# Performance work log

Measured on AMD Instinct MI355X. Metric: run time of the kernel, lower is better.

The kernel has to match this reference:

```python
import jax, jax.numpy as jnp
import numpy as np

EMBED = 256; HEADS = 8; LEVELS = 4; POINTS = 4; HEAD_DIM = EMBED // HEADS
B = 2; Q = 20000; HP = 128; WP = 128
EPS = 1e-5


def setup_inputs() -> dict:
    key = jax.random.key(0)
    ks = jax.random.split(key, 12)
    s = 1.0 / np.sqrt(EMBED)
    return {
        "query": jax.random.normal(ks[0], (Q, EMBED), jnp.float32),
        "query_spatial_positions": jax.random.uniform(ks[1], (Q, 2), jnp.float32),
        "query_batch_offsets": jnp.array([0, Q // 2, Q], dtype=jnp.int32),
        "stacked_feature_maps": jax.random.normal(ks[2], (B, HP, WP, LEVELS, EMBED), jnp.float32),
        "level_spatial_shapes": jnp.array([[128, 128], [64, 64], [32, 32], [16, 16]], dtype=jnp.int32),
        "norm_gamma": jnp.ones((EMBED,), jnp.float32),
        "norm_beta": jnp.zeros((EMBED,), jnp.float32),
        "W_q": jax.random.normal(ks[3], (EMBED, EMBED), jnp.float32) * s,
        "W_off": jax.random.normal(ks[4], (EMBED, HEADS * LEVELS * POINTS * 2), jnp.float32) * s * 0.1,
        "b_off": jax.random.normal(ks[5], (HEADS * LEVELS * POINTS * 2,), jnp.float32) * 0.5,
        "W_attn": jax.random.normal(ks[6], (EMBED, HEADS * LEVELS * POINTS), jnp.float32) * s,
        "b_attn": jnp.zeros((HEADS * LEVELS * POINTS,), jnp.float32),
        "W_val": jax.random.normal(ks[7], (EMBED, EMBED), jnp.float32) * s,
        "b_val": jnp.zeros((EMBED,), jnp.float32),
        "W_out": jax.random.normal(ks[8], (EMBED, EMBED), jnp.float32) * s,
    }


def _layernorm(x, g, b):
    mu = x.mean(-1, keepdims=True)
    xc = x - mu
    v = (xc * xc).mean(-1, keepdims=True)
    return xc * jax.lax.rsqrt(v + EPS) * g + b


def reference(query, query_spatial_positions, query_batch_offsets, stacked_feature_maps,
              level_spatial_shapes, norm_gamma, norm_beta, W_q, W_off, b_off,
              W_attn, b_attn, W_val, b_val, W_out):
    residual = query
    x = _layernorm(query, norm_gamma, norm_beta)
    x = x @ W_q  # q_in_proj (no bias)

    off = (x @ W_off + b_off).reshape(Q, HEADS, LEVELS, POINTS, 2)
    attn = jax.nn.softmax((x @ W_attn + b_attn).reshape(Q, HEADS, LEVELS * POINTS), axis=-1)
    attn = attn.reshape(Q, HEADS, LEVELS, POINTS)

    # value projection over all levels, split into heads: [B,HP,WP,L,H,HD]
    value = (stacked_feature_maps @ W_val + b_val).reshape(B, HP, WP, LEVELS, HEADS, HEAD_DIM)

    shp = level_spatial_shapes.astype(jnp.float32)  # [L,2] (h,w)
    # normalized ref point + offset scaled by level size -> pixel coords (align_corners=False)
    loc = query_spatial_positions[:, None, None, None, :] + off / shp[None, None, :, None, :]
    pix = loc * shp[None, None, :, None, :] - 0.5  # [Q,H,L,P,2]
    py, px = pix[..., 0], pix[..., 1]
    y0 = jnp.floor(py); x0 = jnp.floor(px)
    wy = py - y0; wx = px - x0
    y0i = y0.astype(jnp.int32); x0i = x0.astype(jnp.int32)

    Hl = level_spatial_shapes[:, 0][None, None, :, None]
    Wl = level_spatial_shapes[:, 1][None, None, :, None]
    b_idx = (jnp.searchsorted(query_batch_offsets, jnp.arange(Q, dtype=jnp.int32), side='right') - 1)[:, None, None, None]
    l_idx = jnp.arange(LEVELS)[None, None, :, None]
    h_idx = jnp.arange(HEADS)[None, :, None, None]

    def gather(yi, xi, w):
        m = (yi >= 0) & (yi < Hl) & (xi >= 0) & (xi < Wl)  # zero-pad outside level extent
        yc = jnp.clip(yi, 0, HP - 1)
        xc = jnp.clip(xi, 0, WP - 1)
        v = value[b_idx, yc, xc, l_idx, h_idx]  # [Q,H,L,P,HD]
        return v * (w * m)[..., None]

    samp = (gather(y0i, x0i, (1 - wy) * (1 - wx))
            + gather(y0i, x0i + 1, (1 - wy) * wx)
            + gather(y0i + 1, x0i, wy * (1 - wx))
            + gather(y0i + 1, x0i + 1, wy * wx))

    out = (attn[..., None] * samp).sum(axis=(2, 3)).reshape(Q, EMBED)
    return out @ W_out + residual
```

## Files before the change

kernel.cpp:

```cpp
#include <hip/hip_runtime.h>
#include <hip/hip_bf16.h>
#include <stdint.h>

#define EMBED 256
#define HEADS 8
#define LEVELS 4
#define POINTS 4
#define HEAD_DIM 32
#define HPAD 128
#define WPAD 128
#define LN_EPS 1e-5f

typedef unsigned short u16;
typedef __attribute__((ext_vector_type(8))) short bf16x8v;
typedef __attribute__((ext_vector_type(4))) float f32x4;

static __device__ __forceinline__ float bu2f(u16 u) {
  return __uint_as_float(((unsigned)u) << 16);
}
static __device__ __forceinline__ u16 f2bu(float f) {
  unsigned x = __float_as_uint(f);
  return (u16)((x + 0x7fffu + ((x >> 16) & 1u)) >> 16);
}
static __device__ __forceinline__ float loadf(const void* p, size_t i, int isbf) {
  return isbf ? bu2f(((const u16*)p)[i]) : ((const float*)p)[i];
}
static __device__ __forceinline__ int imin(int a, int b) { return a < b ? a : b; }

static __device__ __forceinline__ void cp16(const u16* g, u16* l) {
  __builtin_amdgcn_global_load_lds((const __attribute__((address_space(1))) unsigned*)g,
                                   (__attribute__((address_space(3))) unsigned*)l, 16, 0, 0);
}

__global__ __launch_bounds__(256) void detect_kernel(const unsigned* __restrict__ q,
                                                     int* __restrict__ flag) {
  int t = threadIdx.x;
  __shared__ int s[256];
  unsigned u = q[t * 13 + 1];
  unsigned e = (u >> 7) & 0xFF;
  s[t] = (e >= 116 && e <= 130) ? 1 : 0;
  __syncthreads();
  for (int st = 128; st > 0; st >>= 1) { if (t < st) s[t] += s[t + st]; __syncthreads(); }
  if (t == 0) *flag = (s[0] > 200) ? 1 : 0;
}

__global__ __launch_bounds__(384) void boa_kernel(const void* __restrict__ b_off,
                                                  const void* __restrict__ b_attn,
                                                  float* __restrict__ boa,
                                                  const int* __restrict__ dflag) {
  int fl = *dflag;
  int t = threadIdx.x;
  boa[t] = (t < 256) ? loadf(b_off, t, fl) : loadf(b_attn, t - 256, fl);
}

__global__ __launch_bounds__(1024) void wcomb_kernel(const void* __restrict__ Wq,
                                                     const void* __restrict__ Woff,
                                                     const void* __restrict__ Wattn,
                                                     u16* __restrict__ Wt,
                                                     const int* __restrict__ dflag) {
  int fl = *dflag;
  int n0 = blockIdx.x * 32, k0 = blockIdx.y * 32;
  int tx = threadIdx.x & 31;
  int ty = threadIdx.x >> 5;
  __shared__ float Aq[32][33];
  __shared__ float Bo[32][33];
  float acc = 0.f;
  for (int j0 = 0; j0 < 256; j0 += 32) {
    Aq[ty][tx] = loadf(Wq, (size_t)(k0 + ty) * 256 + j0 + tx, fl);
    int n = n0 + tx;
    Bo[ty][tx] = (n < 256) ? loadf(Woff,  (size_t)(j0 + ty) * 256 + n,        fl)
                           : loadf(Wattn, (size_t)(j0 + ty) * 128 + (n - 256), fl);
    __syncthreads();
#pragma unroll
    for (int j = 0; j < 32; j++) acc += Aq[ty][j] * Bo[j][tx];
    __syncthreads();
  }
  Wt[(size_t)(n0 + tx) * 256 + k0 + ty] = f2bu(acc);
}

__global__ __launch_bounds__(256) void wtrans_kernel(const void* __restrict__ W,
                                                     u16* __restrict__ Wt,
                                                     int K, int N,
                                                     const int* __restrict__ dflag) {
  int fl = *dflag;
  __shared__ float tile[32][33];
  int tx = threadIdx.x & 31, ty = threadIdx.x >> 5;
  int k0 = blockIdx.x * 32, n0 = blockIdx.y * 32;
#pragma unroll
  for (int j = 0; j < 4; j++) {
    int r = ty + j * 8;
    tile[r][tx] = loadf(W, (size_t)(k0 + r) * N + n0 + tx, fl);
  }
  __syncthreads();
#pragma unroll
  for (int j = 0; j < 4; j++) {
    int n = ty + j * 8;
    Wt[(size_t)(n0 + n) * K + k0 + tx] = f2bu(tile[tx][n]);
  }
}

__global__ __launch_bounds__(256) void ln_kernel(const void* __restrict__ q,
                                                 const void* __restrict__ g,
                                                 const void* __restrict__ be,
                                                 u16* __restrict__ out, int Qn,
                                                 const int* __restrict__ dflag) {
  int fl = *dflag;
  int row = blockIdx.x * 4 + (threadIdx.x >> 6);
  int lane = threadIdx.x & 63;
  if (row >= Qn) return;
  float v0, v1, v2, v3;
  if (fl) {
    uint2 u = *(const uint2*)((const u16*)q + (size_t)row * 256 + lane * 4);
    v0 = bu2f((u16)(u.x & 0xffff)); v1 = bu2f((u16)(u.x >> 16));
    v2 = bu2f((u16)(u.y & 0xffff)); v3 = bu2f((u16)(u.y >> 16));
  } else {
    float4 f = *(const float4*)((const float*)q + (size_t)row * 256 + lane * 4);
    v0 = f.x; v1 = f.y; v2 = f.z; v3 = f.w;
  }
  float s = v0 + v1 + v2 + v3;
#pragma unroll
  for (int m = 1; m < 64; m <<= 1) s += __shfl_xor(s, m, 64);
  float mu = s * (1.f / 256.f);
  float c0 = v0 - mu, c1 = v1 - mu, c2 = v2 - mu, c3 = v3 - mu;
  float s2 = c0 * c0 + c1 * c1 + c2 * c2 + c3 * c3;
#pragma unroll
  for (int m = 1; m < 64; m <<= 1) s2 += __shfl_xor(s2, m, 64);
  float r = rsqrtf(s2 * (1.f / 256.f) + LN_EPS);
  float o0 = c0 * r * loadf(g, lane * 4 + 0, fl) + loadf(be, lane * 4 + 0, fl);
  float o1 = c1 * r * loadf(g, lane * 4 + 1, fl) + loadf(be, lane * 4 + 1, fl);
  float o2 = c2 * r * loadf(g, lane * 4 + 2, fl) + loadf(be, lane * 4 + 2, fl);
  float o3 = c3 * r * loadf(g, lane * 4 + 3, fl) + loadf(be, lane * 4 + 3, fl);
  uint2 w;
  w.x = (unsigned)f2bu(o0) | ((unsigned)f2bu(o1) << 16);
  w.y = (unsigned)f2bu(o2) | ((unsigned)f2bu(o3) << 16);
  *(uint2*)(out + (size_t)row * 256 + lane * 4) = w;
}

template <int OUTMODE, bool ABF>
__global__ __launch_bounds__(256) void mfma_gemm(const void* __restrict__ A,
                                                 const u16* __restrict__ Bt,
                                                 const void* __restrict__ bias, int BiasC,
                                                 const void* __restrict__ resid,
                                                 void* __restrict__ Cv,
                                                 int M, int N, int K,
                                                 const int* __restrict__ dflag) {
  int fl = *dflag;
  __shared__ u16 As[4096];
  __shared__ u16 Bs[4096];
  int tid = threadIdx.x;
  int m0 = blockIdx.x * 128, n0 = blockIdx.y * 128;
  int wave = tid >> 6, lane = tid & 63;
  int quad = lane >> 4, r16 = lane & 15;
  int wm = (wave >> 1) * 64, wn = (wave & 1) * 64;

  f32x4 acc[4][4];
#pragma unroll
  for (int i = 0; i < 4; i++)
#pragma unroll
    for (int j = 0; j < 4; j++) acc[i][j] = (f32x4){0.f, 0.f, 0.f, 0.f};

  int p0 = tid, p1 = tid + 256;
  int r0 = p0 >> 2, c0 = (p0 & 3) * 8;
  int r1 = p1 >> 2, c1 = (p1 & 3) * 8;
  int ra0 = imin(m0 + r0, M - 1), ra1 = imin(m0 + r1, M - 1);

  const u16*   Ab = (const u16*)A;
  const float* Af = (const float*)A;

  for (int k0 = 0; k0 < K; k0 += 32) {
    __syncthreads();
    if (ABF) {
      cp16(Ab + (size_t)ra0 * K + k0 + c0, &As[p0 * 8]);
      cp16(Ab + (size_t)ra1 * K + k0 + c1, &As[p1 * 8]);
    } else if (fl) {
      *(int4*)&As[p0 * 8] = *(const int4*)(Ab + (size_t)ra0 * K + k0 + c0);
      *(int4*)&As[p1 * 8] = *(const int4*)(Ab + (size_t)ra1 * K + k0 + c1);
    } else {
      float4 f00 = *(const float4*)(Af + (size_t)ra0 * K + k0 + c0);
      float4 f01 = *(const float4*)(Af + (size_t)ra0 * K + k0 + c0 + 4);
      float4 f10 = *(const float4*)(Af + (size_t)ra1 * K + k0 + c1);
      float4 f11 = *(const float4*)(Af + (size_t)ra1 * K + k0 + c1 + 4);
      u16* d0 = &As[p0 * 8];
      d0[0] = f2bu(f00.x); d0[1] = f2bu(f00.y); d0[2] = f2bu(f00.z); d0[3] = f2bu(f00.w);
      d0[4] = f2bu(f01.x); d0[5] = f2bu(f01.y); d0[6] = f2bu(f01.z); d0[7] = f2bu(f01.w);
      u16* d1 = &As[p1 * 8];
      d1[0] = f2bu(f10.x); d1[1] = f2bu(f10.y); d1[2] = f2bu(f10.z); d1[3] = f2bu(f10.w);
      d1[4] = f2bu(f11.x); d1[5] = f2bu(f11.y); d1[6] = f2bu(f11.z); d1[7] = f2bu(f11.w);
    }
    cp16(Bt + (size_t)(n0 + r0) * K + k0 + c0, &Bs[p0 * 8]);
    cp16(Bt + (size_t)(n0 + r1) * K + k0 + c1, &Bs[p1 * 8]);
    __syncthreads();

    bf16x8v a[4], b[4];
#pragma unroll
    for (int i = 0; i < 4; i++)
      a[i] = *(const bf16x8v*)&As[(wm + i * 16 + r16) * 32 + quad * 8];
#pragma unroll
    for (int j = 0; j < 4; j++)
      b[j] = *(const bf16x8v*)&Bs[(wn + j * 16 + r16) * 32 + quad * 8];
#pragma unroll
    for (int i = 0; i < 4; i++)
#pragma unroll
      for (int j = 0; j < 4; j++)
        acc[i][j] = __builtin_amdgcn_mfma_f32_16x16x32_bf16(a[i], b[j], acc[i][j], 0, 0, 0);
  }

  int obf = (OUTMODE == 2) ? fl : OUTMODE;
  int bfl = (BiasC == 2) ? fl : 0;
  if (bias) {
#pragma unroll
    for (int j = 0; j < 4; j++) {
      float bv = loadf(bias, n0 + wn + j * 16 + r16, bfl);
#pragma unroll
      for (int i = 0; i < 4; i++)
#pragma unroll
        for (int reg = 0; reg < 4; reg++) acc[i][j][reg] += bv;
    }
  }

  if (obf) {
    int sl0 = (quad << 4) | ((2 * r16) & 15);
    int sl1 = sl0 + 1;
    bool lohalf = (r16 < 8);
#pragma unroll
    for (int i = 0; i < 4; i++) {
#pragma unroll
      for (int jp = 0; jp < 2; jp++) {
#pragma unroll
        for (int reg = 0; reg < 4; reg++) {
          float vA = acc[i][jp * 2][reg], vB = acc[i][jp * 2 + 1][reg];
          float a0 = __shfl(vA, sl0), a1 = __shfl(vA, sl1);
          float b0 = __shfl(vB, sl0), b1 = __shfl(vB, sl1);
          float lo = lohalf ? a0 : b0;
          float hi = lohalf ? a1 : b1;
          int row = m0 + wm + i * 16 + quad * 4 + reg;
          if (row < M) {
            size_t base = (size_t)row * N + n0 + wn + jp * 32 + 2 * r16;
            if (resid) {
              lo += loadf(resid, base, fl);
              hi += loadf(resid, base + 1, fl);
            }
            unsigned pk = (unsigned)f2bu(lo) | ((unsigned)f2bu(hi) << 16);
            *(unsigned*)((u16*)Cv + base) = pk;
          }
        }
      }
    }
  } else {
#pragma unroll
    for (int j = 0; j < 4; j++) {
      int col = n0 + wn + j * 16 + r16;
#pragma unroll
      for (int i = 0; i < 4; i++) {
#pragma unroll
        for (int reg = 0; reg < 4; reg++) {
          int row = m0 + wm + i * 16 + quad * 4 + reg;
          if (row < M) {
            float v = acc[i][j][reg];
            if (resid) v += loadf(resid, (size_t)row * N + col, fl);
            ((float*)Cv)[(size_t)row * N + col] = v;
          }
        }
      }
    }
  }
}

__global__ __launch_bounds__(512) void val_gemm(const void* __restrict__ A,
                                                const u16* __restrict__ Bt,
                                                const void* __restrict__ bias,
                                                u16* __restrict__ Cv,
                                                const int* __restrict__ dflag) {
  int fl = *dflag;
  __shared__ u16 As[128 * 256];
  int tid = threadIdx.x;
  int blk = blockIdx.x;
  int b   = blk / 170;
  int cb  = blk % 170;
  int l, ibase;
  if (cb < 128)      { l = 0; ibase = cb * 128; }
  else if (cb < 160) { l = 1; ibase = (cb - 128) * 128; }
  else if (cb < 168) { l = 2; ibase = (cb - 160) * 128; }
  else               { l = 3; ibase = (cb - 168) * 128; }
  int shift = 7 - l;
  int mask  = (128 >> l) - 1;
  int rowbase = b * 65536 + l;

  int wave = tid >> 6, lane = tid & 63;
  int quad = lane >> 4, r16 = lane & 15;
  int wm = (wave >> 2) * 64, wn = (wave & 3) * 64;

  if (fl) {
    const uint4* A16 = (const uint4*)A;
#pragma unroll
    for (int it = 0; it < 8; it++) {
      int g = it * 512 + tid;
      int r = g >> 5, c = g & 31;
      int i = ibase + r;
      size_t rowg = (size_t)rowbase + (i >> shift) * 512 + (i & mask) * 4;
      uint4 v = A16[rowg * 32 + c];
      *(uint4*)&As[r * 256 + ((c ^ (r & 7)) * 8)] = v;
    }
  } else {
    const float4* A4 = (const float4*)A;
#pragma unroll
    for (int p = 0; p < 2; p++) {
      float4 f[8];
#pragma unroll
      for (int q = 0; q < 8; q++) {
        int g = (p * 8 + q) * 512 + tid;
        int i = ibase + (g >> 6);
        size_t rowg = (size_t)rowbase + (i >> shift) * 512 + (i & mask) * 4;
        f[q] = A4[rowg * 64 + (g & 63)];
      }
#pragma unroll
      for (int q = 0; q < 8; q++) {
        int g = (p * 8 + q) * 512 + tid;
        int r = g >> 6, cw = g & 63;
        int c = cw >> 1, sub = cw & 1;
        uint2 w;
        w.x = (unsigned)f2bu(f[q].x) | ((unsigned)f2bu(f[q].y) << 16);
        w.y = (unsigned)f2bu(f[q].z) | ((unsigned)f2bu(f[q].w) << 16);
        *(uint2*)&As[r * 256 + ((c ^ (r & 7)) * 8) + sub * 4] = w;
      }
    }
  }
  __syncthreads();

  f32x4 acc[4][4];
#pragma unroll
  for (int i = 0; i < 4; i++)
#pragma unroll
    for (int j = 0; j < 4; j++) acc[i][j] = (f32x4){0.f, 0.f, 0.f, 0.f};

  int arow[4], arl[4];
#pragma unroll
  for (int i = 0; i < 4; i++) {
    arow[i] = (wm + i * 16 + r16) * 256;
    arl[i]  = (wm + i * 16 + r16) & 7;
  }
  const u16* bbase[4];
#pragma unroll
  for (int j = 0; j < 4; j++)
    bbase[j] = Bt + (size_t)(wn + j * 16 + r16) * 256 + quad * 8;

#pragma unroll
  for (int t = 0; t < 8; t++) {
    bf16x8v b4[4];
#pragma unroll
    for (int j = 0; j < 4; j++)
      b4[j] = *(const bf16x8v*)(bbase[j] + t * 32);
    bf16x8v a4[4];
#pragma unroll
    for (int i = 0; i < 4; i++) {
      int chunk = ((t << 2) | quad) ^ arl[i];
      a4[i] = *(const bf16x8v*)&As[arow[i] + chunk * 8];
    }
#pragma unroll
    for (int i = 0; i < 4; i++)
#pragma unroll
      for (int j = 0; j < 4; j++)
        acc[i][j] = __builtin_amdgcn_mfma_f32_16x16x32_bf16(a4[i], b4[j], acc[i][j], 0, 0, 0);
  }

#pragma unroll
  for (int j = 0; j < 4; j++) {
    float bv = loadf(bias, wn + j * 16 + r16, fl);
#pragma unroll
    for (int i = 0; i < 4; i++)
#pragma unroll
      for (int reg = 0; reg < 4; reg++) acc[i][j][reg] += bv;
  }
  int sl0 = (quad << 4) | ((2 * r16) & 15);
  int sl1 = sl0 + 1;
  bool lohalf = (r16 < 8);
#pragma unroll
  for (int i = 0; i < 4; i++) {
#pragma unroll
    for (int jp = 0; jp < 2; jp++) {
#pragma unroll
      for (int reg = 0; reg < 4; reg++) {
        float vA = acc[i][jp * 2][reg], vB = acc[i][jp * 2 + 1][reg];
        float a0 = __shfl(vA, sl0), a1 = __shfl(vA, sl1);
        float b0 = __shfl(vB, sl0), b1 = __shfl(vB, sl1);
        float lo = lohalf ? a0 : b0;
        float hi = lohalf ? a1 : b1;
        int rloc = wm + i * 16 + quad * 4 + reg;
        int ii = ibase + rloc;
        size_t rowg = (size_t)rowbase + (ii >> shift) * 512 + (ii & mask) * 4;
        size_t base = rowg * 256 + wn + jp * 32 + 2 * r16;
        unsigned pk = (unsigned)f2bu(lo) | ((unsigned)f2bu(hi) << 16);
        *(unsigned*)(Cv + base) = pk;
      }
    }
  }
}

__global__ __launch_bounds__(256) void sample2_kernel(const float* __restrict__ oa,
                                                      const void* __restrict__ qsp,
                                                      const int* __restrict__ qbo, int nb,
                                                      const int* __restrict__ lss,
                                                      const u16* __restrict__ value,
                                                      u16* __restrict__ samp, int Qn,
                                                      const int* __restrict__ dflag) {
  int fl = *dflag;
  int t = threadIdx.x;
  int q2 = t >> 7;
  int i7 = t & 127;
  int qb = blockIdx.x * 2;
  int q = imin(qb + q2, Qn - 1);

  __shared__ float Loff[2][256];
  __shared__ float Lw[2][128];
  __shared__ int   Lb[2];
  __shared__ int   Co[2][128][4];
  __shared__ float Cw[2][128][4];

  {
    const float* row = oa + (size_t)q * 384;
    float2 v = ((const float2*)row)[i7];
    Loff[q2][i7 * 2]     = v.x;
    Loff[q2][i7 * 2 + 1] = v.y;
    Lw[q2][i7] = row[256 + i7];
  }
  if (t < 2) {
    int qq = imin(qb + t, Qn - 1);
    int b = 0;
    for (int i = 1; i < nb; i++) if (qq >= qbo[i]) b = i;
    Lb[t] = b;
  }
  __syncthreads();

  if (t < 16) {
    int sq = t >> 3, h = t & 7;
    float* w = &Lw[sq][h * 16];
    float mx = w[0];
    for (int i = 1; i < 16; i++) mx = fmaxf(mx, w[i]);
    float s = 0.f;
    for (int i = 0; i < 16; i++) { float e = __expf(w[i] - mx); w[i] = e; s += e; }
    float inv = 1.f / s;
    for (int i = 0; i < 16; i++) w[i] *= inv;
  }
  __syncthreads();

  {
    int h = i7 >> 4, lp = i7 & 15, l = lp >> 2;
    int Hi = lss[l * 2], Wi = lss[l * 2 + 1];
    float Hl = (float)Hi, Wl = (float)Wi;
    float qy = loadf(qsp, (size_t)q * 2, fl);
    float qx = loadf(qsp, (size_t)q * 2 + 1, fl);
    float a  = Lw[q2][i7];
    float oy = Loff[q2][i7 * 2], ox = Loff[q2][i7 * 2 + 1];
    float py = (qy + oy / Hl) * Hl - 0.5f;
    float px = (qx + ox / Wl) * Wl - 0.5f;
    float y0f = floorf(py), x0f = floorf(px);
    float wy = py - y0f, wx = px - x0f;
    int y0 = (int)y0f, x0 = (int)x0f;
    int bbase = Lb[q2] * (HPAD * WPAD * LEVELS * EMBED);
#pragma unroll
    for (int c = 0; c < 4; c++) {
      int yi = y0 + (c >> 1), xi = x0 + (c & 1);
      float w = ((c >> 1) ? wy : 1.f - wy) * ((c & 1) ? wx : 1.f - wx);
      bool ok = (yi >= 0) & (yi < Hi) & (xi >= 0) & (xi < Wi);
      Co[q2][i7][c] = ok ? (bbase + ((yi * WPAD + xi) * LEVELS + l) * EMBED + h * HEAD_DIM) : 0;
      Cw[q2][i7][c] = ok ? (a * w) : 0.f;
    }
  }
  __syncthreads();

  {
    int h = (t >> 4) & 7;
    int d2 = t & 15;
    float ax = 0.f, ay = 0.f;
#pragma unroll
    for (int lp = 0; lp < 16; lp++) {
      int4   o4 = *(const int4*)&Co[q2][h * 16 + lp][0];
      float4 w4 = *(const float4*)&Cw[q2][h * 16 + lp][0];
      unsigned v;
      v = *(const unsigned*)(value + o4.x + d2 * 2);
      ax += w4.x * __uint_as_float(v << 16); ay += w4.x * __uint_as_float(v & 0xffff0000u);
      v = *(const unsigned*)(value + o4.y + d2 * 2);
      ax += w4.y * __uint_as_float(v << 16); ay += w4.y * __uint_as_float(v & 0xffff0000u);
      v = *(const unsigned*)(value + o4.z + d2 * 2);
      ax += w4.z * __uint_as_float(v << 16); ay += w4.z * __uint_as_float(v & 0xffff0000u);
      v = *(const unsigned*)(value + o4.w + d2 * 2);
      ax += w4.w * __uint_as_float(v << 16); ay += w4.w * __uint_as_float(v & 0xffff0000u);
    }
    if (qb + q2 < Qn) {
      unsigned pk = (unsigned)f2bu(ax) | ((unsigned)f2bu(ay) << 16);
      *(unsigned*)(samp + (size_t)(qb + q2) * 256 + h * 32 + d2 * 2) = pk;
    }
  }
}

extern "C" void kernel_launch(void* const* d_in, const int* in_sizes, int n_in,
                              void* d_out, int out_size, void* d_ws, size_t ws_size,
                              hipStream_t stream) {
  const void* query  = d_in[0];
  const void* qsp    = d_in[1];
  const int*  qbo    = (const int*)d_in[2];
  const void* sfm    = d_in[3];
  const int*  lss    = (const int*)d_in[4];
  const void* gamma  = d_in[5];
  const void* beta   = d_in[6];
  const void* W_q    = d_in[7];
  const void* W_off  = d_in[8];
  const void* b_off  = d_in[9];
  const void* W_attn = d_in[10];
  const void* b_attn = d_in[11];
  const void* W_val  = d_in[12];
  const void* b_val  = d_in[13];
  const void* W_out  = d_in[14];

  const int Q  = in_sizes[0] / EMBED;
  const int nb = in_sizes[2] - 1;
  const int MV = in_sizes[3] / EMBED;
  const int B  = MV / (HPAD * WPAD * LEVELS);

  char* ws = (char*)d_ws;
  size_t o = 0;
  auto alloc = [&](size_t bytes) { size_t r = o; o = (o + bytes + 255) & ~(size_t)255; return r; };
  u16*   xln   = (u16*)(ws + alloc((size_t)Q * EMBED * sizeof(u16)));
  float* oaw   = (float*)(ws + alloc((size_t)Q * 384 * sizeof(float)));
  u16*   valw  = (u16*)(ws + alloc((size_t)MV * EMBED * sizeof(u16)));
  u16*   sampw = (u16*)(ws + alloc((size_t)Q * EMBED * sizeof(u16)));
  u16*   wtoa  = (u16*)(ws + alloc(384 * 256 * sizeof(u16)));
  u16*   wtval = (u16*)(ws + alloc(256 * 256 * sizeof(u16)));
  u16*   wtout = (u16*)(ws + alloc(256 * 256 * sizeof(u16)));
  float* boa   = (float*)(ws + alloc(384 * sizeof(float)));
  int*   dflag = (int*)(ws + alloc(256));
  (void)ws_size;

  detect_kernel<<<1, 256, 0, stream>>>((const unsigned*)query, dflag);
  boa_kernel<<<1, 384, 0, stream>>>(b_off, b_attn, boa, dflag);

  wcomb_kernel<<<dim3(12, 8), 1024, 0, stream>>>(W_q, W_off, W_attn, wtoa, dflag);
  wtrans_kernel<<<dim3(8, 8), 256, 0, stream>>>(W_val, wtval, 256, 256, dflag);
  wtrans_kernel<<<dim3(8, 8), 256, 0, stream>>>(W_out, wtout, 256, 256, dflag);

  ln_kernel<<<(Q + 3) / 4, 256, 0, stream>>>(query, gamma, beta, xln, Q, dflag);

  const int GQ = (Q + 127) / 128;
  mfma_gemm<0, true><<<dim3(GQ, 3), 256, 0, stream>>>(xln, wtoa, boa, 0, nullptr, oaw, Q, 384, 256, dflag);
  val_gemm<<<dim3(B * 170), 512, 0, stream>>>(sfm, wtval, b_val, valw, dflag);
  sample2_kernel<<<(Q + 1) / 2, 256, 0, stream>>>(oaw, qsp, qbo, nb, lss, valw, sampw, Q, dflag);
  mfma_gemm<2, true><<<dim3(GQ, 2), 256, 0, stream>>>(sampw, wtout, nullptr, 0, query, d_out, Q, 256, 256, dflag);
}
```

Measured before the change: 375.3 us.

## Fuse LayerNorm into full-K GEMM and fold gamma/beta into weights

LayerNorm is now computed inside the offset/attention GEMM, which loads a full 128x256 A tile into swizzled LDS once and loops over all N blocks. The gamma scale is folded into the combined weight and the beta contribution into the bias via two small precompute kernels. This removes the separate LN kernel and the round trip of its bf16 output through global memory. The output GEMM uses the same full-K kernel. In exchange each block uses 64KB of LDS, which lowers occupancy, B operands are read straight from global memory with no LDS staging, and the fp32 path computes variance as E[x^2]-mu^2.

```diff
diff --git a/kernel.cpp b/kernel.cpp
--- a/kernel.cpp
+++ b/kernel.cpp
@@ -27,11 +27,6 @@
 }
 static __device__ __forceinline__ int imin(int a, int b) { return a < b ? a : b; }
 
-static __device__ __forceinline__ void cp16(const u16* g, u16* l) {
-  __builtin_amdgcn_global_load_lds((const __attribute__((address_space(1))) unsigned*)g,
-                                   (__attribute__((address_space(3))) unsigned*)l, 16, 0, 0);
-}
-
 __global__ __launch_bounds__(256) void detect_kernel(const unsigned* __restrict__ q,
                                                      int* __restrict__ flag) {
   int t = threadIdx.x;
@@ -53,9 +48,34 @@
   boa[t] = (t < 256) ? loadf(b_off, t, fl) : loadf(b_attn, t - 256, fl);
 }
 
+__global__ __launch_bounds__(256) void bfold1_kernel(const void* __restrict__ beta,
+                                                     const void* __restrict__ Wq,
+                                                     float* __restrict__ t1,
+                                                     const int* __restrict__ dflag) {
+  int fl = *dflag;
+  int j = threadIdx.x;
+  float s = 0.f;
+  for (int k = 0; k < 256; k++) s += loadf(beta, k, fl) * loadf(Wq, (size_t)k * 256 + j, fl);
+  t1[j] = s;
+}
+
+__global__ __launch_bounds__(384) void bfold2_kernel(const float* __restrict__ t1,
+                                                     const void* __restrict__ Woff,
+                                                     const void* __restrict__ Wattn,
+                                                     float* __restrict__ boa,
+                                                     const int* __restrict__ dflag) {
+  int fl = *dflag;
+  int n = threadIdx.x;
+  float s = 0.f;
+  if (n < 256) { for (int j = 0; j < 256; j++) s += t1[j] * loadf(Woff,  (size_t)j * 256 + n,        fl); }
+  else         { for (int j = 0; j < 256; j++) s += t1[j] * loadf(Wattn, (size_t)j * 128 + (n - 256), fl); }
+  boa[n] += s;
+}
+
 __global__ __launch_bounds__(1024) void wcomb_kernel(const void* __restrict__ Wq,
                                                      const void* __restrict__ Woff,
                                                      const void* __restrict__ Wattn,
+                                                     const void* __restrict__ gamma,
                                                      u16* __restrict__ Wt,
                                                      const int* __restrict__ dflag) {
   int fl = *dflag;
@@ -75,6 +95,7 @@
     for (int j = 0; j < 32; j++) acc += Aq[ty][j] * Bo[j][tx];
     __syncthreads();
   }
+  acc *= loadf(gamma, k0 + ty, fl);
   Wt[(size_t)(n0 + tx) * 256 + k0 + ty] = f2bu(acc);
 }
 
@@ -99,143 +120,163 @@
   }
 }
 
-__global__ __launch_bounds__(256) void ln_kernel(const void* __restrict__ q,
-                                                 const void* __restrict__ g,
-                                                 const void* __restrict__ be,
-                                                 u16* __restrict__ out, int Qn,
-                                                 const int* __restrict__ dflag) {
-  int fl = *dflag;
-  int row = blockIdx.x * 4 + (threadIdx.x >> 6);
-  int lane = threadIdx.x & 63;
-  if (row >= Qn) return;
-  float v0, v1, v2, v3;
-  if (fl) {
-    uint2 u = *(const uint2*)((const u16*)q + (size_t)row * 256 + lane * 4);
-    v0 = bu2f((u16)(u.x & 0xffff)); v1 = bu2f((u16)(u.x >> 16));
-    v2 = bu2f((u16)(u.y & 0xffff)); v3 = bu2f((u16)(u.y >> 16));
-  } else {
-    float4 f = *(const float4*)((const float*)q + (size_t)row * 256 + lane * 4);
-    v0 = f.x; v1 = f.y; v2 = f.z; v3 = f.w;
-  }
-  float s = v0 + v1 + v2 + v3;
-#pragma unroll
-  for (int m = 1; m < 64; m <<= 1) s += __shfl_xor(s, m, 64);
-  float mu = s * (1.f / 256.f);
-  float c0 = v0 - mu, c1 = v1 - mu, c2 = v2 - mu, c3 = v3 - mu;
-  float s2 = c0 * c0 + c1 * c1 + c2 * c2 + c3 * c3;
-#pragma unroll
-  for (int m = 1; m < 64; m <<= 1) s2 += __shfl_xor(s2, m, 64);
-  float r = rsqrtf(s2 * (1.f / 256.f) + LN_EPS);
-  float o0 = c0 * r * loadf(g, lane * 4 + 0, fl) + loadf(be, lane * 4 + 0, fl);
-  float o1 = c1 * r * loadf(g, lane * 4 + 1, fl) + loadf(be, lane * 4 + 1, fl);
-  float o2 = c2 * r * loadf(g, lane * 4 + 2, fl) + loadf(be, lane * 4 + 2, fl);
-  float o3 = c3 * r * loadf(g, lane * 4 + 3, fl) + loadf(be, lane * 4 + 3, fl);
-  uint2 w;
-  w.x = (unsigned)f2bu(o0) | ((unsigned)f2bu(o1) << 16);
-  w.y = (unsigned)f2bu(o2) | ((unsigned)f2bu(o3) << 16);
-  *(uint2*)(out + (size_t)row * 256 + lane * 4) = w;
-}
-
-template <int OUTMODE, bool ABF>
-__global__ __launch_bounds__(256) void mfma_gemm(const void* __restrict__ A,
-                                                 const u16* __restrict__ Bt,
-                                                 const void* __restrict__ bias, int BiasC,
-                                                 const void* __restrict__ resid,
-                                                 void* __restrict__ Cv,
-                                                 int M, int N, int K,
-                                                 const int* __restrict__ dflag) {
-  int fl = *dflag;
-  __shared__ u16 As[4096];
-  __shared__ u16 Bs[4096];
+template <int OUTMODE, bool DOLN>
+__global__ __launch_bounds__(512) void fullk_gemm(const void* __restrict__ A,
+                                                  const u16* __restrict__ Bt,
+                                                  const float* __restrict__ bias,
+                                                  const void* __restrict__ resid,
+                                                  void* __restrict__ Cv,
+                                                  int M, int NB,
+                                                  const int* __restrict__ dflag) {
+  int fl = *dflag;
+  __shared__ u16 As[128 * 256];
   int tid = threadIdx.x;
-  int m0 = blockIdx.x * 128, n0 = blockIdx.y * 128;
+  int m0 = blockIdx.x * 128;
   int wave = tid >> 6, lane = tid & 63;
   int quad = lane >> 4, r16 = lane & 15;
-  int wm = (wave >> 1) * 64, wn = (wave & 1) * 64;
-
-  f32x4 acc[4][4];
-#pragma unroll
-  for (int i = 0; i < 4; i++)
-#pragma unroll
-    for (int j = 0; j < 4; j++) acc[i][j] = (f32x4){0.f, 0.f, 0.f, 0.f};
-
-  int p0 = tid, p1 = tid + 256;
-  int r0 = p0 >> 2, c0 = (p0 & 3) * 8;
-  int r1 = p1 >> 2, c1 = (p1 & 3) * 8;
-  int ra0 = imin(m0 + r0, M - 1), ra1 = imin(m0 + r1, M - 1);
-
-  const u16*   Ab = (const u16*)A;
-  const float* Af = (const float*)A;
-
-  for (int k0 = 0; k0 < K; k0 += 32) {
-    __syncthreads();
-    if (ABF) {
-      cp16(Ab + (size_t)ra0 * K + k0 + c0, &As[p0 * 8]);
-      cp16(Ab + (size_t)ra1 * K + k0 + c1, &As[p1 * 8]);
-    } else if (fl) {
-      *(int4*)&As[p0 * 8] = *(const int4*)(Ab + (size_t)ra0 * K + k0 + c0);
-      *(int4*)&As[p1 * 8] = *(const int4*)(Ab + (size_t)ra1 * K + k0 + c1);
+  int wm = (wave >> 2) * 64, wn = (wave & 3) * 32;
+  const int N = NB * 128;
+
+  if (DOLN) {
+    int r = tid >> 2, qt = tid & 3;
+    int ra = imin(m0 + r, M - 1);
+    if (fl) {
+      uint4 d[8];
+      const uint4* Ar = (const uint4*)((const u16*)A + (size_t)ra * 256 + qt * 64);
+#pragma unroll
+      for (int i = 0; i < 8; i++) d[i] = Ar[i];
+      float s = 0.f;
+#pragma unroll
+      for (int i = 0; i < 8; i++) {
+        unsigned w0 = d[i].x, w1 = d[i].y, w2 = d[i].z, w3 = d[i].w;
+        s += __uint_as_float(w0 << 16) + __uint_as_float(w0 & 0xffff0000u)
+           + __uint_as_float(w1 << 16) + __uint_as_float(w1 & 0xffff0000u)
+           + __uint_as_float(w2 << 16) + __uint_as_float(w2 & 0xffff0000u)
+           + __uint_as_float(w3 << 16) + __uint_as_float(w3 & 0xffff0000u);
+      }
+      s += __shfl_xor(s, 1, 64); s += __shfl_xor(s, 2, 64);
+      float mu = s * (1.f / 256.f);
+      float sq = 0.f;
+#pragma unroll
+      for (int i = 0; i < 8; i++) {
+        unsigned w0 = d[i].x, w1 = d[i].y, w2 = d[i].z, w3 = d[i].w;
+        float c;
+        c = __uint_as_float(w0 << 16) - mu; sq += c * c;
+        c = __uint_as_float(w0 & 0xffff0000u) - mu; sq += c * c;
+        c = __uint_as_float(w1 << 16) - mu; sq += c * c;
+        c = __uint_as_float(w1 & 0xffff0000u) - mu; sq += c * c;
+        c = __uint_as_float(w2 << 16) - mu; sq += c * c;
+        c = __uint_as_float(w2 & 0xffff0000u) - mu; sq += c * c;
+        c = __uint_as_float(w3 << 16) - mu; sq += c * c;
+        c = __uint_as_float(w3 & 0xffff0000u) - mu; sq += c * c;
+      }
+      sq += __shfl_xor(sq, 1, 64); sq += __shfl_xor(sq, 2, 64);
+      float rr = rsqrtf(sq * (1.f / 256.f) + LN_EPS);
+#pragma unroll
+      for (int i = 0; i < 8; i++) {
+        unsigned w[4] = {d[i].x, d[i].y, d[i].z, d[i].w};
+        uint4 o;
+        unsigned* op = &o.x;
+#pragma unroll
+        for (int k = 0; k < 4; k++) {
+          float lo = (__uint_as_float(w[k] << 16) - mu) * rr;
+          float hi = (__uint_as_float(w[k] & 0xffff0000u) - mu) * rr;
+          op[k] = (unsigned)f2bu(lo) | ((unsigned)f2bu(hi) << 16);
+        }
+        int c = qt * 8 + i;
+        *(uint4*)&As[r * 256 + ((c ^ (r & 7)) * 8)] = o;
+      }
     } else {
-      float4 f00 = *(const float4*)(Af + (size_t)ra0 * K + k0 + c0);
-      float4 f01 = *(const float4*)(Af + (size_t)ra0 * K + k0 + c0 + 4);
-      float4 f10 = *(const float4*)(Af + (size_t)ra1 * K + k0 + c1);
-      float4 f11 = *(const float4*)(Af + (size_t)ra1 * K + k0 + c1 + 4);
-      u16* d0 = &As[p0 * 8];
-      d0[0] = f2bu(f00.x); d0[1] = f2bu(f00.y); d0[2] = f2bu(f00.z); d0[3] = f2bu(f00.w);
-      d0[4] = f2bu(f01.x); d0[5] = f2bu(f01.y); d0[6] = f2bu(f01.z); d0[7] = f2bu(f01.w);
-      u16* d1 = &As[p1 * 8];
-      d1[0] = f2bu(f10.x); d1[1] = f2bu(f10.y); d1[2] = f2bu(f10.z); d1[3] = f2bu(f10.w);
-      d1[4] = f2bu(f11.x); d1[5] = f2bu(f11.y); d1[6] = f2bu(f11.z); d1[7] = f2bu(f11.w);
-    }
-    cp16(Bt + (size_t)(n0 + r0) * K + k0 + c0, &Bs[p0 * 8]);
-    cp16(Bt + (size_t)(n0 + r1) * K + k0 + c1, &Bs[p1 * 8]);
-    __syncthreads();
-
-    bf16x8v a[4], b[4];
-#pragma unroll
-    for (int i = 0; i < 4; i++)
-      a[i] = *(const bf16x8v*)&As[(wm + i * 16 + r16) * 32 + quad * 8];
-#pragma unroll
-    for (int j = 0; j < 4; j++)
-      b[j] = *(const bf16x8v*)&Bs[(wn + j * 16 + r16) * 32 + quad * 8];
-#pragma unroll
-    for (int i = 0; i < 4; i++)
-#pragma unroll
-      for (int j = 0; j < 4; j++)
-        acc[i][j] = __builtin_amdgcn_mfma_f32_16x16x32_bf16(a[i], b[j], acc[i][j], 0, 0, 0);
+      const float4* Ar4 = (const float4*)((const float*)A + (size_t)ra * 256 + qt * 64);
+      float s = 0.f, sq = 0.f;
+#pragma unroll
+      for (int i = 0; i < 16; i++) {
+        float4 f = Ar4[i];
+        s  += f.x + f.y + f.z + f.w;
+        sq += f.x * f.x + f.y * f.y + f.z * f.z + f.w * f.w;
+      }
+      s  += __shfl_xor(s, 1, 64);  s  += __shfl_xor(s, 2, 64);
+      sq += __shfl_xor(sq, 1, 64); sq += __shfl_xor(sq, 2, 64);
+      float mu = s * (1.f / 256.f);
+      float var = sq * (1.f / 256.f) - mu * mu;
+      float rr = rsqrtf(fmaxf(var, 0.f) + LN_EPS);
+#pragma unroll
+      for (int i = 0; i < 16; i += 2) {
+        float4 f0 = Ar4[i], f1 = Ar4[i + 1];
+        uint4 o;
+        o.x = (unsigned)f2bu((f0.x - mu) * rr) | ((unsigned)f2bu((f0.y - mu) * rr) << 16);
+        o.y = (unsigned)f2bu((f0.z - mu) * rr) | ((unsigned)f2bu((f0.w - mu) * rr) << 16);
+        o.z = (unsigned)f2bu((f1.x - mu) * rr) | ((unsigned)f2bu((f1.y - mu) * rr) << 16);
+        o.w = (unsigned)f2bu((f1.z - mu) * rr) | ((unsigned)f2bu((f1.w - mu) * rr) << 16);
+        int c = qt * 8 + (i >> 1);
+        *(uint4*)&As[r * 256 + ((c ^ (r & 7)) * 8)] = o;
+      }
+    }
+  } else {
+    const uint4* A16 = (const uint4*)A;
+#pragma unroll
+    for (int it = 0; it < 8; it++) {
+      int g = it * 512 + tid;
+      int r = g >> 5, c = g & 31;
+      int ra = imin(m0 + r, M - 1);
+      uint4 v = A16[(size_t)ra * 32 + c];
+      *(uint4*)&As[r * 256 + ((c ^ (r & 7)) * 8)] = v;
+    }
+  }
+  __syncthreads();
+
+  int arow[4], arl[4];
+#pragma unroll
+  for (int i = 0; i < 4; i++) {
+    int rw = wm + i * 16 + r16;
+    arow[i] = rw * 256;
+    arl[i]  = rw & 7;
   }
 
   int obf = (OUTMODE == 2) ? fl : OUTMODE;
-  int bfl = (BiasC == 2) ? fl : 0;
-  if (bias) {
-#pragma unroll
-    for (int j = 0; j < 4; j++) {
-      float bv = loadf(bias, n0 + wn + j * 16 + r16, bfl);
+  int sl0 = (quad << 4) | ((2 * r16) & 15);
+  int sl1 = sl0 + 1;
+  bool lohalf = (r16 < 8);
+
+  for (int nb = 0; nb < NB; ++nb) {
+    f32x4 acc[4][2];
+#pragma unroll
+    for (int i = 0; i < 4; i++) { acc[i][0] = (f32x4){0.f,0.f,0.f,0.f}; acc[i][1] = (f32x4){0.f,0.f,0.f,0.f}; }
+    const u16* bb0 = Bt + (size_t)(nb * 128 + wn + r16) * 256 + quad * 8;
+    const u16* bb1 = bb0 + 16 * 256;
+#pragma unroll
+    for (int t = 0; t < 8; t++) {
+      bf16x8v b0 = *(const bf16x8v*)(bb0 + t * 32);
+      bf16x8v b1 = *(const bf16x8v*)(bb1 + t * 32);
+#pragma unroll
+      for (int i = 0; i < 4; i++) {
+        int chunk = ((t << 2) | quad) ^ arl[i];
+        bf16x8v a = *(const bf16x8v*)&As[arow[i] + chunk * 8];
+        acc[i][0] = __builtin_amdgcn_mfma_f32_16x16x32_bf16(a, b0, acc[i][0], 0, 0, 0);
+        acc[i][1] = __builtin_amdgcn_mfma_f32_16x16x32_bf16(a, b1, acc[i][1], 0, 0, 0);
+      }
+    }
+    if (bias) {
+      float bv0 = bias[nb * 128 + wn + r16];
+      float bv1 = bias[nb * 128 + wn + 16 + r16];
 #pragma unroll
       for (int i = 0; i < 4; i++)
 #pragma unroll
-        for (int reg = 0; reg < 4; reg++) acc[i][j][reg] += bv;
-    }
-  }
-
-  if (obf) {
-    int sl0 = (quad << 4) | ((2 * r16) & 15);
-    int sl1 = sl0 + 1;
-    bool lohalf = (r16 < 8);
-#pragma unroll
-    for (int i = 0; i < 4; i++) {
-#pragma unroll
-      for (int jp = 0; jp < 2; jp++) {
+        for (int reg = 0; reg < 4; reg++) { acc[i][0][reg] += bv0; acc[i][1][reg] += bv1; }
+    }
+    if (obf) {
+#pragma unroll
+      for (int i = 0; i < 4; i++) {
 #pragma unroll
         for (int reg = 0; reg < 4; reg++) {
-          float vA = acc[i][jp * 2][reg], vB = acc[i][jp * 2 + 1][reg];
+          float vA = acc[i][0][reg], vB = acc[i][1][reg];
           float a0 = __shfl(vA, sl0), a1 = __shfl(vA, sl1);
-          float b0 = __shfl(vB, sl0), b1 = __shfl(vB, sl1);
-          float lo = lohalf ? a0 : b0;
-          float hi = lohalf ? a1 : b1;
+          float b0s = __shfl(vB, sl0), b1s = __shfl(vB, sl1);
+          float lo = lohalf ? a0 : b0s;
+          float hi = lohalf ? a1 : b1s;
           int row = m0 + wm + i * 16 + quad * 4 + reg;
           if (row < M) {
-            size_t base = (size_t)row * N + n0 + wn + jp * 32 + 2 * r16;
+            size_t base = (size_t)row * N + nb * 128 + wn + 2 * r16;
             if (resid) {
               lo += loadf(resid, base, fl);
               hi += loadf(resid, base + 1, fl);
@@ -245,20 +286,20 @@
           }
         }
       }
-    }
-  } else {
-#pragma unroll
-    for (int j = 0; j < 4; j++) {
-      int col = n0 + wn + j * 16 + r16;
-#pragma unroll
-      for (int i = 0; i < 4; i++) {
-#pragma unroll
-        for (int reg = 0; reg < 4; reg++) {
-          int row = m0 + wm + i * 16 + quad * 4 + reg;
-          if (row < M) {
-            float v = acc[i][j][reg];
-            if (resid) v += loadf(resid, (size_t)row * N + col, fl);
-            ((float*)Cv)[(size_t)row * N + col] = v;
+    } else {
+#pragma unroll
+      for (int j = 0; j < 2; j++) {
+        int col = nb * 128 + wn + j * 16 + r16;
+#pragma unroll
+        for (int i = 0; i < 4; i++) {
+#pragma unroll
+          for (int reg = 0; reg < 4; reg++) {
+            int row = m0 + wm + i * 16 + quad * 4 + reg;
+            if (row < M) {
+              float v = acc[i][j][reg];
+              if (resid) v += loadf(resid, (size_t)row * N + col, fl);
+              ((float*)Cv)[(size_t)row * N + col] = v;
+            }
           }
         }
       }
@@ -520,7 +561,6 @@
   char* ws = (char*)d_ws;
   size_t o = 0;
   auto alloc = [&](size_t bytes) { size_t r = o; o = (o + bytes + 255) & ~(size_t)255; return r; };
-  u16*   xln   = (u16*)(ws + alloc((size_t)Q * EMBED * sizeof(u16)));
   float* oaw   = (float*)(ws + alloc((size_t)Q * 384 * sizeof(float)));
   u16*   valw  = (u16*)(ws + alloc((size_t)MV * EMBED * sizeof(u16)));
   u16*   sampw = (u16*)(ws + alloc((size_t)Q * EMBED * sizeof(u16)));
@@ -528,21 +568,22 @@
   u16*   wtval = (u16*)(ws + alloc(256 * 256 * sizeof(u16)));
   u16*   wtout = (u16*)(ws + alloc(256 * 256 * sizeof(u16)));
   float* boa   = (float*)(ws + alloc(384 * sizeof(float)));
+  float* t1    = (float*)(ws + alloc(256 * sizeof(float)));
   int*   dflag = (int*)(ws + alloc(256));
   (void)ws_size;
 
   detect_kernel<<<1, 256, 0, stream>>>((const unsigned*)query, dflag);
   boa_kernel<<<1, 384, 0, stream>>>(b_off, b_attn, boa, dflag);
-
-  wcomb_kernel<<<dim3(12, 8), 1024, 0, stream>>>(W_q, W_off, W_attn, wtoa, dflag);
+  bfold1_kernel<<<1, 256, 0, stream>>>(beta, W_q, t1, dflag);
+  bfold2_kernel<<<1, 384, 0, stream>>>(t1, W_off, W_attn, boa, dflag);
+
+  wcomb_kernel<<<dim3(12, 8), 1024, 0, stream>>>(W_q, W_off, W_attn, gamma, wtoa, dflag);
   wtrans_kernel<<<dim3(8, 8), 256, 0, stream>>>(W_val, wtval, 256, 256, dflag);
   wtrans_kernel<<<dim3(8, 8), 256, 0, stream>>>(W_out, wtout, 256, 256, dflag);
 
-  ln_kernel<<<(Q + 3) / 4, 256, 0, stream>>>(query, gamma, beta, xln, Q, dflag);
-
   const int GQ = (Q + 127) / 128;
-  mfma_gemm<0, true><<<dim3(GQ, 3), 256, 0, stream>>>(xln, wtoa, boa, 0, nullptr, oaw, Q, 384, 256, dflag);
+  fullk_gemm<0, true><<<GQ, 512, 0, stream>>>(query, wtoa, boa, nullptr, oaw, Q, 3, dflag);
   val_gemm<<<dim3(B * 170), 512, 0, stream>>>(sfm, wtval, b_val, valw, dflag);
   sample2_kernel<<<(Q + 1) / 2, 256, 0, stream>>>(oaw, qsp, qbo, nb, lss, valw, sampw, Q, dflag);
-  mfma_gemm<2, true><<<dim3(GQ, 2), 256, 0, stream>>>(sampw, wtout, nullptr, 0, query, d_out, Q, 256, 256, dflag);
-}
+  fullk_gemm<2, false><<<GQ, 512, 0, stream>>>(sampw, wtout, nullptr, query, d_out, Q, 2, dflag);
+}
```

Result: slower. 464.2 us (+23.7%).
